# Kernel optimization log

Hardware: AMD Instinct MI355X
Metric: run time of the kernel (lower is better)

The kernel has to match this reference:

```python
import jax, jax.numpy as jnp
import numpy as np

B, N, E = 8, 4096, 65536
FIN, OUT, T, H = 128, 128, 4, 4
C = OUT // H  # per-head channels
NEG_SLOPE = 0.2
EPS_LN = 1e-5


def setup_inputs() -> dict:
    key = jax.random.key(0)
    ks = jax.random.split(key, 10)
    x = jax.random.normal(ks[0], (B, N, FIN), dtype=jnp.float32)
    edge_index = jax.random.randint(ks[1], (B, 2, E), 0, N, dtype=jnp.int64)
    edge_type = jax.random.randint(ks[2], (B, E), 0, T, dtype=jnp.int64)
    # per-edge-type GATConv params (PyG GATConv: lin weight, att_src, att_dst, bias)
    W = jax.random.normal(ks[3], (T, FIN, H * C), dtype=jnp.float32) / np.sqrt(FIN)
    a_src = jax.random.normal(ks[4], (T, H, C), dtype=jnp.float32) / np.sqrt(C)
    a_dst = jax.random.normal(ks[5], (T, H, C), dtype=jnp.float32) / np.sqrt(C)
    bias = jnp.zeros((T, H * C), dtype=jnp.float32)
    gamma = jnp.ones((OUT,), dtype=jnp.float32)
    beta = jnp.zeros((OUT,), dtype=jnp.float32)
    return {"x": x, "edge_index": edge_index, "edge_type": edge_type,
            "W": W, "a_src": a_src, "a_dst": a_dst, "bias": bias,
            "gamma": gamma, "beta": beta}


def _gat_aggregate(h, src, dst, mask):
    """Single-graph masked GAT aggregation.
    h: [N,H,C] transformed features; src,dst: [E]; mask: [E] bool.
    Returns [N,H,C].
    """
    n = h.shape[0]
    a_s = h[src]                     # [E,H,C] source features (messages)
    # attention logits: att_src . h_src + att_dst . h_dst, done by caller via h-dot
    return a_s, n


def reference(x, edge_index, edge_type, W, a_src, a_dst, bias, gamma, beta):
    b, n, _ = x.shape
    src = edge_index[:, 0, :]  # [B,E]
    dst = edge_index[:, 1, :]

    def per_graph(e_logit, src_b, dst_b, mask_b, h_b):
        # e_logit: [E,H]; h_b: [N,H,C]
        e_m = jnp.where(mask_b[:, None], e_logit, -1e30)
        m = jax.ops.segment_max(e_m, dst_b, num_segments=n)      # [N,H]
        m = jnp.maximum(m, -1e30)
        ex = jnp.exp(e_m - m[dst_b]) * mask_b[:, None]           # [E,H]
        den = jax.ops.segment_sum(ex, dst_b, num_segments=n)     # [N,H]
        alpha = ex / (den[dst_b] + 1e-16)                        # [E,H]
        msg = alpha[:, :, None] * h_b[src_b]                     # [E,H,C]
        return jax.ops.segment_sum(msg, dst_b, num_segments=n)   # [N,H,C]

    out = jnp.zeros((b, n, H * C), dtype=x.dtype)
    for t in range(T):
        h = jnp.einsum('bnf,fo->bno', x, W[t]).reshape(b, n, H, C)
        al_s = jnp.einsum('bnhc,hc->bnh', h, a_src[t])           # [B,N,H]
        al_d = jnp.einsum('bnhc,hc->bnh', h, a_dst[t])
        e = jax.nn.leaky_relu(
            jnp.take_along_axis(al_s, src[..., None], axis=1) +
            jnp.take_along_axis(al_d, dst[..., None], axis=1),
            negative_slope=NEG_SLOPE)                            # [B,E,H]
        mask = (edge_type == t)
        agg = jax.vmap(per_graph)(e, src, dst, mask, h)          # [B,N,H,C]
        out = out + agg.reshape(b, n, H * C) + bias[t]
    # residual + LayerNorm (dropout is identity in eval)
    y = x + out
    mu = jnp.mean(y, axis=-1, keepdims=True)
    var = jnp.var(y, axis=-1, keepdims=True)
    return (y - mu) / jnp.sqrt(var + EPS_LN) * gamma + beta
```

## Files before the change

### kernel.cpp

```cpp
#include <hip/hip_runtime.h>

typedef unsigned int uint;
typedef unsigned short ushort;
typedef __attribute__((ext_vector_type(8))) short short8;
typedef __attribute__((ext_vector_type(4))) float f32x4;

#define Bb 8
#define Nn 4096
#define Ee 65536
#define Tt 4

__device__ __forceinline__ ushort bf16_rne_u(float f) {
    uint u = __float_as_uint(f);
    u += 0x7FFFu + ((u >> 16) & 1u);
    return (ushort)(u >> 16);
}

__global__ __launch_bounds__(256) void fused_a_kernel(
    const int* __restrict__ ei, const int* __restrict__ et, uint* __restrict__ count,
    const float* __restrict__ W, const float* __restrict__ a_src,
    const float* __restrict__ a_dst, ushort* __restrict__ Wf,
    const float* __restrict__ bias, float* __restrict__ bias_sum)
{
    int bid = blockIdx.x;
    int tid = threadIdx.x;
    if (bid < 2048) {
        int i = bid * 256 + tid;
        int b = i >> 16;
        int e = i & (Ee - 1);
        int dst = ei[(size_t)b * 2 * Ee + Ee + e];
        int t = et[(size_t)b * Ee + e];
        atomicAdd(&count[(((uint)(b * Nn + dst)) << 2) | (uint)t], 1u);
    } else if (bid < 2084) {
        int gid = (bid - 2048) * 256 + tid;
        int t    = gid / 2304;
        int rem  = gid % 2304;
        int ks   = rem / 576;
        int rem2 = rem % 576;
        int nt   = rem2 >> 6;
        int lane = rem2 & 63;
        int nl = lane & 15;
        int g  = lane >> 4;
        int k0 = ks * 32 + 4 * g;
        const float* Wt = W + t * 16384;
        union { uint4 q; ushort u[8]; } P;
        if (nt < 8) {
            int n = nt * 16 + nl;
#pragma unroll
            for (int j = 0; j < 4; ++j) P.u[j]     = bf16_rne_u(Wt[(size_t)(k0 + j) * 128 + n]);
#pragma unroll
            for (int j = 0; j < 4; ++j) P.u[4 + j] = bf16_rne_u(Wt[(size_t)(k0 + 16 + j) * 128 + n]);
        } else if (nl < 8) {
            const float* av = (nl < 4) ? a_src : a_dst;
            const float* ah = av + t * 128 + (nl & 3) * 32;
#pragma unroll
            for (int j = 0; j < 8; ++j) {
                int k = k0 + (j < 4 ? j : 12 + j);
                const float* wr = Wt + (size_t)k * 128 + (nl & 3) * 32;
                float s = 0.f;
#pragma unroll 8
                for (int c = 0; c < 32; ++c) s += wr[c] * ah[c];
                P.u[j] = bf16_rne_u(s);
            }
        } else {
            P.q = make_uint4(0u, 0u, 0u, 0u);
        }
        *reinterpret_cast<uint4*>(Wf + ((size_t)((t * 4 + ks) * 9 + nt) * 64 + lane) * 8) = P.q;
    } else {
        if (tid < 128)
            bias_sum[tid] = bias[tid] + bias[128 + tid] + bias[256 + tid] + bias[384 + tid];
    }
}

__global__ __launch_bounds__(256, 4) void fused_b_kernel(
    const float* __restrict__ x, const ushort* __restrict__ Wf,
    ushort* __restrict__ h, float* __restrict__ al_s, float* __restrict__ al_d,
    const uint* __restrict__ cnt, uint* __restrict__ offs, uint* __restrict__ bsum)
{
    __shared__ ushort Hst[4][1024];

    int tid = threadIdx.x;

    if (blockIdx.x >= 1024) {
        uint* ws = reinterpret_cast<uint*>(&Hst[0][0]);
        int cblk = blockIdx.x - 1024;
        int lane = tid & 63, wv = tid >> 6;
        uint4 c = reinterpret_cast<const uint4*>(cnt)[cblk * 256 + tid];
        uint tot = c.x + c.y + c.z + c.w;
        uint inc = tot;
#pragma unroll
        for (int d = 1; d < 64; d <<= 1) {
            uint tv = (uint)__shfl_up((int)inc, d);
            if (lane >= d) inc += tv;
        }
        if (lane == 63) ws[wv] = inc;
        __syncthreads();
        uint wexcl = 0;
        for (int w = 0; w < wv; ++w) wexcl += ws[w];
        uint P = wexcl + inc - tot;
        uint4 o;
        o.x = P; o.y = P + c.x; o.z = o.y + c.y; o.w = o.z + c.z;
        reinterpret_cast<uint4*>(offs)[cblk * 256 + tid] = o;
        if (tid == 255) bsum[cblk] = P + tot;
        return;
    }

    int blk    = blockIdx.x;
    int b      = blk >> 7;
    int rowblk = blk & 127;
    int w    = tid >> 6;
    int lane = tid & 63;
    int nl = lane & 15;
    int g  = lane >> 4;
    int rg  = w & 1;
    int chn = w >> 1;
    int row0 = rowblk * 32 + rg * 16;
    ushort* hw = Hst[w];

    short8 Ah[4], Al[4];
    {
        const float* xr = x + ((size_t)b * Nn + row0 + nl) * 128;
#pragma unroll
        for (int ks = 0; ks < 4; ++ks) {
            float4 fa = *reinterpret_cast<const float4*>(xr + ks * 32 + 4 * g);
            float4 fb = *reinterpret_cast<const float4*>(xr + ks * 32 + 16 + 4 * g);
            float v[8] = {fa.x, fa.y, fa.z, fa.w, fb.x, fb.y, fb.z, fb.w};
            union { short8 s; ushort u[8]; } H, L;
#pragma unroll
            for (int j = 0; j < 8; ++j) {
                ushort hi = bf16_rne_u(v[j]);
                float fh = __uint_as_float(((uint)hi) << 16);
                H.u[j] = hi;
                L.u[j] = bf16_rne_u(v[j] - fh);
            }
            Ah[ks] = H.s;
            Al[ks] = L.s;
        }
    }

    const uint4* Wfq = reinterpret_cast<const uint4*>(Wf);

    for (int t = 0; t < Tt; ++t) {
        f32x4 acc[4];
#pragma unroll
        for (int i = 0; i < 4; ++i) acc[i] = (f32x4){0.f, 0.f, 0.f, 0.f};
        f32x4 acc_al = (f32x4){0.f, 0.f, 0.f, 0.f};

#pragma unroll
        for (int ks = 0; ks < 4; ++ks) {
            union { uint4 q; short8 s; } F[4], Fa;
#pragma unroll
            for (int i = 0; i < 4; ++i)
                F[i].q = Wfq[((t * 4 + ks) * 9 + chn * 4 + i) * 64 + lane];
            if (w < 2)
                Fa.q = Wfq[((t * 4 + ks) * 9 + 8) * 64 + lane];
#pragma unroll
            for (int i = 0; i < 4; ++i) {
                acc[i] = __builtin_amdgcn_mfma_f32_16x16x32_bf16(Ah[ks], F[i].s, acc[i], 0, 0, 0);
                acc[i] = __builtin_amdgcn_mfma_f32_16x16x32_bf16(Al[ks], F[i].s, acc[i], 0, 0, 0);
            }
            if (w < 2) {
                acc_al = __builtin_amdgcn_mfma_f32_16x16x32_bf16(Ah[ks], Fa.s, acc_al, 0, 0, 0);
                acc_al = __builtin_amdgcn_mfma_f32_16x16x32_bf16(Al[ks], Fa.s, acc_al, 0, 0, 0);
            }
        }

        if (w < 2 && nl < 8) {
            int head = nl & 3;
            float* ap = (nl < 4 ? al_s : al_d)
                      + ((size_t)(b * Tt + t) * Nn + row0 + 4 * g) * 4 + head;
#pragma unroll
            for (int r = 0; r < 4; ++r) ap[4 * r] = acc_al[r];
        }

#pragma unroll
        for (int i = 0; i < 4; ++i) {
#pragma unroll
            for (int r = 0; r < 4; ++r) {
                int rowl  = 4 * g + r;
                int colws = i * 16 + nl;
                hw[rowl * 64 + (colws ^ ((rowl & 3) << 3))] = bf16_rne_u(acc[i][r]);
            }
        }

        {
            ushort* hb = h + ((size_t)(b * Tt + t) * Nn + row0) * 128 + chn * 64;
#pragma unroll
            for (int p = 0; p < 2; ++p) {
                int task = p * 64 + lane;
                int rowl = task >> 3;
                int c8   = (task & 7) * 8;
                uint4 v = *reinterpret_cast<const uint4*>(&hw[rowl * 64 + (c8 ^ ((rowl & 3) << 3))]);
                *reinterpret_cast<uint4*>(hb + (size_t)rowl * 128 + c8) = v;
            }
        }
    }
}

__global__ __launch_bounds__(256) void scatter_lr_kernel(
    const int* __restrict__ ei, const int* __restrict__ et,
    const float* __restrict__ al_s, const float* __restrict__ al_d,
    const uint* __restrict__ offs, const uint* __restrict__ bsum,
    uint* __restrict__ cursor, uint* __restrict__ src_sorted, float4* __restrict__ lr_sorted)
{
    __shared__ uint bsx_l[128];
    int tid = threadIdx.x;
    if (tid < 64) {
        uint v0 = bsum[2 * tid], v1 = bsum[2 * tid + 1];
        uint s = v0 + v1, inc = s;
#pragma unroll
        for (int d = 1; d < 64; d <<= 1) {
            uint tv = (uint)__shfl_up((int)inc, d);
            if (tid >= d) inc += tv;
        }
        uint excl = inc - s;
        bsx_l[2 * tid] = excl;
        bsx_l[2 * tid + 1] = excl + v0;
    }
    __syncthreads();

    int i = blockIdx.x * 256 + tid;
    int b = i >> 16;
    int e = i & (Ee - 1);
    int src = ei[(size_t)b * 2 * Ee + e];
    int dst = ei[(size_t)b * 2 * Ee + Ee + e];
    int t = et[(size_t)b * Ee + e];
    uint g = (((uint)(b * Nn + dst)) << 2) | (uint)t;
    uint slot = atomicAdd(&cursor[g], 1u);
    uint p = offs[g] + bsx_l[g >> 10] + slot;

    size_t btN = (size_t)(b * Tt + t) * Nn;
    float4 s4 = *reinterpret_cast<const float4*>(&al_s[(btN + src) * 4]);
    float4 d4 = *reinterpret_cast<const float4*>(&al_d[(btN + dst) * 4]);
    float4 lr;
    lr.x = s4.x + d4.x; lr.x = lr.x > 0.f ? lr.x : 0.2f * lr.x;
    lr.y = s4.y + d4.y; lr.y = lr.y > 0.f ? lr.y : 0.2f * lr.y;
    lr.z = s4.z + d4.z; lr.z = lr.z > 0.f ? lr.z : 0.2f * lr.z;
    lr.w = s4.w + d4.w; lr.w = lr.w > 0.f ? lr.w : 0.2f * lr.w;
    src_sorted[p] = (uint)src;
    lr_sorted[p] = lr;
}

__global__ __launch_bounds__(256) void gat_ln_kernel(
    const float* __restrict__ x, const ushort* __restrict__ h,
    const uint* __restrict__ count, const uint* __restrict__ offs, const uint* __restrict__ bsum,
    const uint* __restrict__ src_sorted, const float4* __restrict__ lr_sorted,
    const float* __restrict__ bias_sum, const float* __restrict__ gamma, const float* __restrict__ beta,
    float* __restrict__ out)
{
    __shared__ uint  su_s[16][96];
    __shared__ float ew_s[16][96 * 4];
    __shared__ uint  bsx_l[128];

    int tid = threadIdx.x;
    if (tid < 64) {
        uint v0 = bsum[2 * tid], v1 = bsum[2 * tid + 1];
        uint s = v0 + v1, inc = s;
#pragma unroll
        for (int d = 1; d < 64; d <<= 1) {
            uint tv = (uint)__shfl_up((int)inc, d);
            if (tid >= d) inc += tv;
        }
        uint excl = inc - s;
        bsx_l[2 * tid] = excl;
        bsx_l[2 * tid + 1] = excl + v0;
    }
    __syncthreads();

    int wl   = tid >> 6;
    int lane = tid & 63;
    int ng = lane >> 4;
    int cl = lane & 15;
    int c0 = cl << 3;
    int hh = cl >> 2;
    int grp = wl * 4 + ng;
    uint*  su = su_s[grp];
    float* ew = ew_s[grp];

    int wid = blockIdx.x * 16 + grp;
    int b   = wid >> 12;
    int dst = wid & (Nn - 1);

    uint4 cnt4 = reinterpret_cast<const uint4*>(count)[wid];
    uint4 off4 = reinterpret_cast<const uint4*>(offs)[wid];
    uint base  = off4.x + bsx_l[((uint)wid) >> 8];
    uint D     = min(off4.w + cnt4.w - off4.x, 96u);

    for (uint i = cl; i < D; i += 16) {
        float4 l4 = lr_sorted[base + i];
        su[i] = src_sorted[base + i];
        ew[i * 4 + 0] = __expf(l4.x);
        ew[i * 4 + 1] = __expf(l4.y);
        ew[i * 4 + 2] = __expf(l4.z);
        ew[i * 4 + 3] = __expf(l4.w);
    }
    __syncthreads();

    uint rel[4] = {0u, off4.y - off4.x, off4.z - off4.x, off4.w - off4.x};
    uint ctv[4] = {cnt4.x, cnt4.y, cnt4.z, cnt4.w};

    float tot[8];
#pragma unroll
    for (int k = 0; k < 8; ++k) tot[k] = 0.f;

#pragma unroll
    for (int t = 0; t < Tt; ++t) {
        uint ct = ctv[t];
        if (!ct) continue;
        uint p0 = rel[t];
        const ushort* hs = h + (size_t)(b * Tt + t) * Nn * 128;

        float acc[8];
#pragma unroll
        for (int k = 0; k < 8; ++k) acc[k] = 0.f;
        float den = 0.f;

        for (uint j = 0; j < ct; ++j) {
            uint i = p0 + j;
            float aw = ew[i * 4 + hh];
            uint  sj = su[i];
            uint4 hv = *reinterpret_cast<const uint4*>(hs + (size_t)sj * 128 + c0);
            float f0 = __uint_as_float(hv.x << 16);
            float f1 = __uint_as_float(hv.x & 0xFFFF0000u);
            float f2 = __uint_as_float(hv.y << 16);
            float f3 = __uint_as_float(hv.y & 0xFFFF0000u);
            float f4 = __uint_as_float(hv.z << 16);
            float f5 = __uint_as_float(hv.z & 0xFFFF0000u);
            float f6 = __uint_as_float(hv.w << 16);
            float f7 = __uint_as_float(hv.w & 0xFFFF0000u);
            acc[0] += aw * f0; acc[1] += aw * f1;
            acc[2] += aw * f2; acc[3] += aw * f3;
            acc[4] += aw * f4; acc[5] += aw * f5;
            acc[6] += aw * f6; acc[7] += aw * f7;
            den += aw;
        }
        float rden = 1.f / (den + 1e-16f);
#pragma unroll
        for (int k = 0; k < 8; ++k) tot[k] += acc[k] * rden;
    }

    size_t obase = ((size_t)b * Nn + dst) * 128 + c0;
    float y[8];
    {
        float4 xa = *reinterpret_cast<const float4*>(x + obase);
        float4 xb = *reinterpret_cast<const float4*>(x + obase + 4);
        float4 ba = *reinterpret_cast<const float4*>(bias_sum + c0);
        float4 bb = *reinterpret_cast<const float4*>(bias_sum + c0 + 4);
        y[0] = xa.x + tot[0] + ba.x; y[1] = xa.y + tot[1] + ba.y;
        y[2] = xa.z + tot[2] + ba.z; y[3] = xa.w + tot[3] + ba.w;
        y[4] = xb.x + tot[4] + bb.x; y[5] = xb.y + tot[5] + bb.y;
        y[6] = xb.z + tot[6] + bb.z; y[7] = xb.w + tot[7] + bb.w;
    }

    float s = 0.f, ss = 0.f;
#pragma unroll
    for (int k = 0; k < 8; ++k) { s += y[k]; ss += y[k] * y[k]; }
#pragma unroll
    for (int off = 1; off < 16; off <<= 1) {
        s += __shfl_xor(s, off);
        ss += __shfl_xor(ss, off);
    }
    float mu = s * (1.f / 128.f);
    float var = ss * (1.f / 128.f) - mu * mu;
    float rstd = rsqrtf(var + 1e-5f);

    float4 ga = *reinterpret_cast<const float4*>(gamma + c0);
    float4 gb = *reinterpret_cast<const float4*>(gamma + c0 + 4);
    float4 ea = *reinterpret_cast<const float4*>(beta + c0);
    float4 eb = *reinterpret_cast<const float4*>(beta + c0 + 4);
    float4 o1, o2;
    o1.x = (y[0] - mu) * rstd * ga.x + ea.x;
    o1.y = (y[1] - mu) * rstd * ga.y + ea.y;
    o1.z = (y[2] - mu) * rstd * ga.z + ea.z;
    o1.w = (y[3] - mu) * rstd * ga.w + ea.w;
    o2.x = (y[4] - mu) * rstd * gb.x + eb.x;
    o2.y = (y[5] - mu) * rstd * gb.y + eb.y;
    o2.z = (y[6] - mu) * rstd * gb.z + eb.z;
    o2.w = (y[7] - mu) * rstd * gb.w + eb.w;
    *reinterpret_cast<float4*>(out + obase) = o1;
    *reinterpret_cast<float4*>(out + obase + 4) = o2;
}

extern "C" void kernel_launch(void* const* d_in, const int* in_sizes, int n_in,
                              void* d_out, int out_size, void* d_ws, size_t ws_size,
                              hipStream_t stream)
{
    const float* x     = (const float*)d_in[0];
    const int*   ei    = (const int*)d_in[1];
    const int*   et    = (const int*)d_in[2];
    const float* W     = (const float*)d_in[3];
    const float* a_src = (const float*)d_in[4];
    const float* a_dst = (const float*)d_in[5];
    const float* bias  = (const float*)d_in[6];
    const float* gamma = (const float*)d_in[7];
    const float* beta  = (const float*)d_in[8];
    float* out = (float*)d_out;

    ushort* h   = (ushort*)d_ws;
    size_t hsz  = (size_t)Bb * Tt * Nn * 128;
    float* al_s = (float*)(h + hsz);
    size_t alsz = (size_t)Bb * Tt * Nn * 4;
    float* al_d = al_s + alsz;
    uint* count  = (uint*)(al_d + alsz);
    uint* cursor = count + (size_t)Bb * Tt * Nn;
    uint* offs   = cursor + (size_t)Bb * Tt * Nn;
    uint* bsum   = offs + (size_t)Bb * Tt * Nn;
    float* bias_sum = (float*)(bsum + 128);
    uint* src_sorted = (uint*)(bias_sum + 128);
    float4* lr_sorted = (float4*)(src_sorted + (size_t)Bb * Ee);
    ushort* Wf = (ushort*)(lr_sorted + (size_t)Bb * Ee);

    hipMemsetAsync(count, 0, (size_t)Bb * Tt * Nn * 2 * sizeof(uint), stream);

    fused_a_kernel<<<2085, 256, 0, stream>>>(ei, et, count, W, a_src, a_dst, Wf, bias, bias_sum);
    fused_b_kernel<<<1152, 256, 0, stream>>>(x, Wf, h, al_s, al_d, count, offs, bsum);
    scatter_lr_kernel<<<(Bb * Ee) / 256, 256, 0, stream>>>(
        ei, et, al_s, al_d, offs, bsum, cursor, src_sorted, lr_sorted);
    gat_ln_kernel<<<(Bb * Nn) / 16, 256, 0, stream>>>(
        x, h, count, offs, bsum, src_sorted, lr_sorted, bias_sum, gamma, beta, out);
}
```

Before: 180.1 us.

## Drop bf16 split-precision MFMA and compute edge logits in aggregation kernel

The x projection no longer uses a hi/lo bf16 split with two MFMAs per tile. It now uses a single bf16 MFMA, halving the matrix work in fused_b but lowering precision of h and the attention logits. Separately, the scatter kernel no longer gathers al_s/al_d or writes a sorted float4 logit array. The aggregation kernel instead recovers the edge type from the segment offsets and gathers the logit terms itself. This removes one global write/read of per-edge logits at the cost of random gathers in the final kernel.

```diff
diff --git a/kernel.cpp b/kernel.cpp
--- a/kernel.cpp
+++ b/kernel.cpp
@@ -117,7 +117,7 @@
     int row0 = rowblk * 32 + rg * 16;
     ushort* hw = Hst[w];
 
-    short8 Ah[4], Al[4];
+    short8 Ah[4];
     {
         const float* xr = x + ((size_t)b * Nn + row0 + nl) * 128;
 #pragma unroll
@@ -125,16 +125,10 @@
             float4 fa = *reinterpret_cast<const float4*>(xr + ks * 32 + 4 * g);
             float4 fb = *reinterpret_cast<const float4*>(xr + ks * 32 + 16 + 4 * g);
             float v[8] = {fa.x, fa.y, fa.z, fa.w, fb.x, fb.y, fb.z, fb.w};
-            union { short8 s; ushort u[8]; } H, L;
-#pragma unroll
-            for (int j = 0; j < 8; ++j) {
-                ushort hi = bf16_rne_u(v[j]);
-                float fh = __uint_as_float(((uint)hi) << 16);
-                H.u[j] = hi;
-                L.u[j] = bf16_rne_u(v[j] - fh);
-            }
+            union { short8 s; ushort u[8]; } H;
+#pragma unroll
+            for (int j = 0; j < 8; ++j) H.u[j] = bf16_rne_u(v[j]);
             Ah[ks] = H.s;
-            Al[ks] = L.s;
         }
     }
 
@@ -155,14 +149,10 @@
             if (w < 2)
                 Fa.q = Wfq[((t * 4 + ks) * 9 + 8) * 64 + lane];
 #pragma unroll
-            for (int i = 0; i < 4; ++i) {
+            for (int i = 0; i < 4; ++i)
                 acc[i] = __builtin_amdgcn_mfma_f32_16x16x32_bf16(Ah[ks], F[i].s, acc[i], 0, 0, 0);
-                acc[i] = __builtin_amdgcn_mfma_f32_16x16x32_bf16(Al[ks], F[i].s, acc[i], 0, 0, 0);
-            }
-            if (w < 2) {
+            if (w < 2)
                 acc_al = __builtin_amdgcn_mfma_f32_16x16x32_bf16(Ah[ks], Fa.s, acc_al, 0, 0, 0);
-                acc_al = __builtin_amdgcn_mfma_f32_16x16x32_bf16(Al[ks], Fa.s, acc_al, 0, 0, 0);
-            }
         }
 
         if (w < 2 && nl < 8) {
@@ -197,11 +187,10 @@
     }
 }
 
-__global__ __launch_bounds__(256) void scatter_lr_kernel(
+__global__ __launch_bounds__(256) void scatter_kernel(
     const int* __restrict__ ei, const int* __restrict__ et,
-    const float* __restrict__ al_s, const float* __restrict__ al_d,
     const uint* __restrict__ offs, const uint* __restrict__ bsum,
-    uint* __restrict__ cursor, uint* __restrict__ src_sorted, float4* __restrict__ lr_sorted)
+    uint* __restrict__ cursor, uint* __restrict__ src_sorted)
 {
     __shared__ uint bsx_l[128];
     int tid = threadIdx.x;
@@ -228,23 +217,14 @@
     uint g = (((uint)(b * Nn + dst)) << 2) | (uint)t;
     uint slot = atomicAdd(&cursor[g], 1u);
     uint p = offs[g] + bsx_l[g >> 10] + slot;
-
-    size_t btN = (size_t)(b * Tt + t) * Nn;
-    float4 s4 = *reinterpret_cast<const float4*>(&al_s[(btN + src) * 4]);
-    float4 d4 = *reinterpret_cast<const float4*>(&al_d[(btN + dst) * 4]);
-    float4 lr;
-    lr.x = s4.x + d4.x; lr.x = lr.x > 0.f ? lr.x : 0.2f * lr.x;
-    lr.y = s4.y + d4.y; lr.y = lr.y > 0.f ? lr.y : 0.2f * lr.y;
-    lr.z = s4.z + d4.z; lr.z = lr.z > 0.f ? lr.z : 0.2f * lr.z;
-    lr.w = s4.w + d4.w; lr.w = lr.w > 0.f ? lr.w : 0.2f * lr.w;
     src_sorted[p] = (uint)src;
-    lr_sorted[p] = lr;
 }
 
 __global__ __launch_bounds__(256) void gat_ln_kernel(
     const float* __restrict__ x, const ushort* __restrict__ h,
     const uint* __restrict__ count, const uint* __restrict__ offs, const uint* __restrict__ bsum,
-    const uint* __restrict__ src_sorted, const float4* __restrict__ lr_sorted,
+    const uint* __restrict__ src_sorted,
+    const float* __restrict__ al_s, const float* __restrict__ al_d,
     const float* __restrict__ bias_sum, const float* __restrict__ gamma, const float* __restrict__ beta,
     float* __restrict__ out)
 {
@@ -286,17 +266,27 @@
     uint base  = off4.x + bsx_l[((uint)wid) >> 8];
     uint D     = min(off4.w + cnt4.w - off4.x, 96u);
 
+    uint r1 = off4.y - off4.x, r2 = off4.z - off4.x, r3 = off4.w - off4.x;
+
     for (uint i = cl; i < D; i += 16) {
-        float4 l4 = lr_sorted[base + i];
-        su[i] = src_sorted[base + i];
-        ew[i * 4 + 0] = __expf(l4.x);
-        ew[i * 4 + 1] = __expf(l4.y);
-        ew[i * 4 + 2] = __expf(l4.z);
-        ew[i * 4 + 3] = __expf(l4.w);
+        uint src = src_sorted[base + i];
+        int t = (int)(i >= r1) + (int)(i >= r2) + (int)(i >= r3);
+        size_t slab = (size_t)(b * Tt + t) * Nn;
+        float4 s4 = *reinterpret_cast<const float4*>(&al_s[(slab + src) * 4]);
+        float4 d4 = *reinterpret_cast<const float4*>(&al_d[(slab + dst) * 4]);
+        float lx = s4.x + d4.x; lx = lx > 0.f ? lx : 0.2f * lx;
+        float ly = s4.y + d4.y; ly = ly > 0.f ? ly : 0.2f * ly;
+        float lz = s4.z + d4.z; lz = lz > 0.f ? lz : 0.2f * lz;
+        float lw = s4.w + d4.w; lw = lw > 0.f ? lw : 0.2f * lw;
+        su[i] = src;
+        ew[i * 4 + 0] = __expf(lx);
+        ew[i * 4 + 1] = __expf(ly);
+        ew[i * 4 + 2] = __expf(lz);
+        ew[i * 4 + 3] = __expf(lw);
     }
     __syncthreads();
 
-    uint rel[4] = {0u, off4.y - off4.x, off4.z - off4.x, off4.w - off4.x};
+    uint rel[4] = {0u, r1, r2, r3};
     uint ctv[4] = {cnt4.x, cnt4.y, cnt4.z, cnt4.w};
 
     float tot[8];
@@ -407,15 +397,14 @@
     uint* bsum   = offs + (size_t)Bb * Tt * Nn;
     float* bias_sum = (float*)(bsum + 128);
     uint* src_sorted = (uint*)(bias_sum + 128);
-    float4* lr_sorted = (float4*)(src_sorted + (size_t)Bb * Ee);
-    ushort* Wf = (ushort*)(lr_sorted + (size_t)Bb * Ee);
+    ushort* Wf = (ushort*)(src_sorted + (size_t)Bb * Ee);
 
     hipMemsetAsync(count, 0, (size_t)Bb * Tt * Nn * 2 * sizeof(uint), stream);
 
     fused_a_kernel<<<2085, 256, 0, stream>>>(ei, et, count, W, a_src, a_dst, Wf, bias, bias_sum);
     fused_b_kernel<<<1152, 256, 0, stream>>>(x, Wf, h, al_s, al_d, count, offs, bsum);
-    scatter_lr_kernel<<<(Bb * Ee) / 256, 256, 0, stream>>>(
-        ei, et, al_s, al_d, offs, bsum, cursor, src_sorted, lr_sorted);
+    scatter_kernel<<<(Bb * Ee) / 256, 256, 0, stream>>>(
+        ei, et, offs, bsum, cursor, src_sorted);
     gat_ln_kernel<<<(Bb * Nn) / 16, 256, 0, stream>>>(
-        x, h, count, offs, bsum, src_sorted, lr_sorted, bias_sum, gamma, beta, out);
-}
+        x, h, count, offs, bsum, src_sorted, al_s, al_d, bias_sum, gamma, beta, out);
+}
```

Result: no change. 178.8 us (-0.7%).
